# Performance work log

Measured on AMD Instinct MI355X. Metric: run time of the kernel, lower is better.

## Reference

```python
import jax, jax.numpy as jnp
import numpy as np

CHUNK_SIZE = 1024  # module default chunk_size


def setup_inputs() -> dict:
    key = jax.random.key(0)
    kq, kk, kv = jax.random.split(key, 3)
    B, H, S, D = 2, 16, 2048, 64
    q = jax.random.normal(kq, (B, H, S, D), dtype=jnp.float32)
    k = jax.random.normal(kk, (B, H, S, D), dtype=jnp.float32)
    v = jax.random.normal(kv, (B, H, S, D), dtype=jnp.float32)
    return {"q": q, "k": k, "v": v}


def reference(q, k, v):
    # Chunked causal attention: q split into chunks of CHUNK_SIZE along seq,
    # each chunk attends to the full K/V with causal mask (tril, diagonal=start).
    B, H, S, D = q.shape
    scale = D ** (-0.5)
    cs = CHUNK_SIZE
    nc = S // cs  # S is a multiple of chunk_size here
    qc = q.reshape(B, H, nc, cs, D)
    # scores: [B, H, nc, cs, S]
    scores = jnp.einsum('bhncd,bhsd->bhncs', qc, k) * scale
    # causal mask per chunk: key position j visible iff j <= chunk_start + i
    row = (jnp.arange(nc) * cs)[:, None, None] + jnp.arange(cs)[None, :, None]  # [nc, cs, 1]
    col = jnp.arange(S)[None, None, :]  # [1, 1, S]
    causal = col <= row  # [nc, cs, S]
    scores = jnp.where(causal[None, None], scores, -jnp.inf)
    attn = jax.nn.softmax(scores, axis=-1)
    out = jnp.einsum('bhncs,bhsd->bhncd', attn, v)
    return out.reshape(B, H, S, D)
```

## Files before the change

kernel.cpp:

```cpp
#include <hip/hip_runtime.h>

typedef __bf16 bf16x8 __attribute__((ext_vector_type(8)));
typedef float f32x4 __attribute__((ext_vector_type(4)));
typedef float f32x16 __attribute__((ext_vector_type(16)));

#define S_LEN 2048
#define D_DIM 64
#define NHEAD 32
#define PART_FLOATS 8448

typedef __attribute__((address_space(1))) const void gas;
typedef __attribute__((address_space(3))) void las;

#define J(c, t0, nt) ((unsigned short)((c) | ((t0) << 4) | ((nt) << 9)))
__device__ const unsigned short TRIP[24] = {
    J(15,0,16), J(15,16,16), J(0,0,2),
    J(7,0,16),  J(13,0,14),  J(1,0,4),
    J(14,0,15), J(12,0,13),  J(2,0,6),
    J(14,15,15),J(10,0,11),  J(3,0,8),
    J(13,14,14),J(10,11,11), J(8,0,9),
    J(6,0,14),  J(9,0,10),   J(9,10,10),
    J(12,13,13),J(11,0,12),  J(8,9,9),
    J(11,12,12),J(5,0,12),   J(4,0,10),
};

__global__ __launch_bounds__(256) void convert_kv(const float* __restrict__ K,
                                                  const float* __restrict__ V,
                                                  __bf16* __restrict__ Kb,
                                                  __bf16* __restrict__ Vtg) {
    const int head = blockIdx.y;
    const int s0   = blockIdx.x * 64;
    const int tr   = threadIdx.x >> 2;
    const int tc   = (threadIdx.x & 3) << 4;
    const size_t ib = (size_t)head * (S_LEN * D_DIM) + (size_t)(s0 + tr) * D_DIM + tc;

    __shared__ __bf16 tb[64][72];

    {
        const float* kr = K + ib;
        f32x4 a = *(const f32x4*)kr, b = *(const f32x4*)(kr + 4),
              c = *(const f32x4*)(kr + 8), d = *(const f32x4*)(kr + 12);
        bf16x8 o0, o1;
        #pragma unroll
        for (int e = 0; e < 4; ++e) {
            o0[e] = (__bf16)a[e]; o0[e + 4] = (__bf16)b[e];
            o1[e] = (__bf16)c[e]; o1[e + 4] = (__bf16)d[e];
        }
        __bf16* ko = Kb + ib;
        *(bf16x8*)ko = o0; *(bf16x8*)(ko + 8) = o1;
    }
    {
        const float* vr = V + ib;
        f32x4 a = *(const f32x4*)vr, b = *(const f32x4*)(vr + 4),
              c = *(const f32x4*)(vr + 8), d = *(const f32x4*)(vr + 12);
        #pragma unroll
        for (int e = 0; e < 4; ++e) {
            tb[tc +  e][tr] = (__bf16)a[e];
            tb[tc + 4 + e][tr] = (__bf16)b[e];
            tb[tc + 8 + e][tr] = (__bf16)c[e];
            tb[tc + 12 + e][tr] = (__bf16)d[e];
        }
    }
    __syncthreads();
    {
        bf16x8 o0, o1;
        #pragma unroll
        for (int e = 0; e < 8; ++e) { o0[e] = tb[tr][tc + e]; o1[e] = tb[tr][tc + 8 + e]; }
        __bf16* vo = Vtg + (size_t)head * (D_DIM * S_LEN) + (size_t)tr * S_LEN + s0 + tc;
        *(bf16x8*)vo = o0; *(bf16x8*)(vo + 8) = o1;
    }
}

__global__ __launch_bounds__(256, 3) void attn32(const float* __restrict__ Q,
                                                 const __bf16* __restrict__ Kb,
                                                 const __bf16* __restrict__ Vg,
                                                 float* __restrict__ O,
                                                 float* __restrict__ Pp) {
    const int b    = blockIdx.x;
    const int xcd  = b & 7;
    const int cu   = (b >> 3) & 31;
    const int pass = b >> 8;
    const int head = xcd * 4 + (cu >> 3);
    const unsigned short jw = TRIP[(cu & 7) * 3 + pass];
    const int chunk = jw & 15;
    const int t0    = (jw >> 4) & 31;
    const int nt    = jw >> 9;

    const int tid  = threadIdx.x;
    const int wave = tid >> 6;
    const int lane = tid & 63;
    const int l31  = lane & 31;
    const int hi   = lane >> 5;
    const int sw31 = (l31 & 7) << 3;

    const int q0w = chunk * 128 + wave * 32;
    const size_t qbase = (size_t)head * (S_LEN * D_DIM);
    const size_t vbase = (size_t)head * (D_DIM * S_LEN);
    const float qscale = 0.125f * 1.44269504088896340736f;

    __shared__ __align__(16) __bf16 Klds[2][64][64];
    __shared__ __align__(16) __bf16 Vt[2][64][64];

    const int xsw = (lane & 7) ^ ((lane >> 3) & 7);
    const size_t kOff = (size_t)(lane >> 3) * D_DIM + (size_t)xsw * 8;
    const size_t vOff = (size_t)(lane >> 3) * S_LEN + (size_t)xsw * 8;
    const __bf16* kgw = Kb + qbase + (size_t)(wave * 16) * D_DIM + kOff;
    const __bf16* vgw = Vg + vbase + (size_t)(wave * 16) * S_LEN + vOff;

    bf16x8 qf[4];
    {
        const float* qrow = Q + qbase + (size_t)(q0w + l31) * D_DIM + hi * 8;
        #pragma unroll
        for (int kd = 0; kd < 4; ++kd) {
            f32x4 a = *(const f32x4*)(qrow + kd * 16);
            f32x4 c = *(const f32x4*)(qrow + kd * 16 + 4);
            bf16x8 t;
            #pragma unroll
            for (int e = 0; e < 4; ++e) { t[e] = (__bf16)(a[e] * qscale); t[e + 4] = (__bf16)(c[e] * qscale); }
            qf[kd] = t;
        }
    }

    f32x16 acc0 = {0.f}, acc1 = {0.f};
    #pragma unroll
    for (int r = 0; r < 16; ++r) { acc0[r] = 0.f; acc1[r] = 0.f; }
    float m_r = -1e30f, l_r = 0.f;

    auto stage = [&](int kv0, int bufi) {
        const __bf16* kg = kgw + (size_t)kv0 * D_DIM;
        const __bf16* vg = vgw + kv0;
        __builtin_amdgcn_global_load_lds((gas*)kg,               (las*)&Klds[bufi][wave * 16][0],     16, 0, 0);
        __builtin_amdgcn_global_load_lds((gas*)(kg + 8 * D_DIM), (las*)&Klds[bufi][wave * 16 + 8][0], 16, 0, 0);
        __builtin_amdgcn_global_load_lds((gas*)vg,               (las*)&Vt[bufi][wave * 16][0],       16, 0, 0);
        __builtin_amdgcn_global_load_lds((gas*)(vg + 8 * S_LEN), (las*)&Vt[bufi][wave * 16 + 8][0],   16, 0, 0);
    };
    auto cvtpk = [](float lo, float hh) {
        unsigned int r;
        asm("v_cvt_pk_bf16_f32 %0, %1, %2" : "=v"(r) : "v"(lo), "v"(hh));
        return r;
    };

    stage(t0 << 6, 0);

    for (int it = 0; it < nt; ++it) {
        const int cur = it & 1;
        asm volatile("s_waitcnt vmcnt(0)" ::: "memory");
        __syncthreads();

        if (it + 1 < nt) stage((t0 + it + 1) << 6, cur ^ 1);
        const int kv0 = (t0 + it) << 6;

        if (kv0 <= q0w + 31) {
            f32x16 s0, s1;
            #pragma unroll
            for (int r = 0; r < 16; ++r) { s0[r] = 0.f; s1[r] = 0.f; }
            __builtin_amdgcn_s_setprio(1);
            #pragma unroll
            for (int kd = 0; kd < 4; ++kd) {
                bf16x8 kf0 = *(const bf16x8*)&Klds[cur][l31][(kd * 16 + hi * 8) ^ sw31];
                bf16x8 kf1 = *(const bf16x8*)&Klds[cur][32 + l31][(kd * 16 + hi * 8) ^ sw31];
                s0 = __builtin_amdgcn_mfma_f32_32x32x16_bf16(kf0, qf[kd], s0, 0, 0, 0);
                s1 = __builtin_amdgcn_mfma_f32_32x32x16_bf16(kf1, qf[kd], s1, 0, 0, 0);
            }
            __builtin_amdgcn_s_setprio(0);

            if (kv0 + 63 > q0w) {
                const int qg = q0w + l31;
                #pragma unroll
                for (int r = 0; r < 16; ++r) {
                    const int cr = (r & 3) + 8 * (r >> 2) + 4 * hi;
                    if (kv0 + cr > qg)      s0[r] = -1e30f;
                    if (kv0 + 32 + cr > qg) s1[r] = -1e30f;
                }
            }

            float mm = -1e30f;
            #pragma unroll
            for (int r = 0; r < 16; ++r) mm = fmaxf(mm, fmaxf(s0[r], s1[r]));
            mm = fmaxf(mm, __shfl_xor(mm, 32));
            if (!__all(mm - m_r <= 8.0f)) {
                const float mn = fmaxf(m_r, mm);
                const float f = exp2f(m_r - mn);
                m_r = mn;
                l_r *= f;
                #pragma unroll
                for (int r = 0; r < 16; ++r) {
                    const float fr = __shfl(f, (r & 3) + 8 * (r >> 2) + 4 * hi);
                    acc0[r] *= fr; acc1[r] *= fr;
                }
            }
            float ps = 0.f, ps2 = 0.f;
            #pragma unroll
            for (int r = 0; r < 16; ++r) {
                s0[r] = exp2f(s0[r] - m_r); ps  += s0[r];
                s1[r] = exp2f(s1[r] - m_r); ps2 += s1[r];
            }
            ps += ps2;
            ps += __shfl_xor(ps, 32);
            l_r += ps;

            __builtin_amdgcn_s_setprio(1);
            {
                unsigned int w01 = cvtpk(s0[0],  s0[1]),  w23 = cvtpk(s0[2],  s0[3]);
                unsigned int w45 = cvtpk(s0[4],  s0[5]),  w67 = cvtpk(s0[6],  s0[7]);
                unsigned int w89 = cvtpk(s0[8],  s0[9]),  wab = cvtpk(s0[10], s0[11]);
                unsigned int wcd = cvtpk(s0[12], s0[13]), wef = cvtpk(s0[14], s0[15]);
                asm("v_permlane32_swap_b32 %0, %1" : "+v"(w01), "+v"(w45));
                asm("v_permlane32_swap_b32 %0, %1" : "+v"(w23), "+v"(w67));
                asm("v_permlane32_swap_b32 %0, %1" : "+v"(w89), "+v"(wcd));
                asm("v_permlane32_swap_b32 %0, %1" : "+v"(wab), "+v"(wef));
                union { unsigned int u[4]; bf16x8 v; } f0 = {{w01, w23, w45, w67}};
                union { unsigned int u[4]; bf16x8 v; } f1 = {{w89, wab, wcd, wef}};
                bf16x8 v00 = *(const bf16x8*)&Vt[cur][l31][(hi * 8) ^ sw31];
                bf16x8 v01 = *(const bf16x8*)&Vt[cur][32 + l31][(hi * 8) ^ sw31];
                acc0 = __builtin_amdgcn_mfma_f32_32x32x16_bf16(f0.v, v00, acc0, 0, 0, 0);
                acc1 = __builtin_amdgcn_mfma_f32_32x32x16_bf16(f0.v, v01, acc1, 0, 0, 0);
                bf16x8 v10 = *(const bf16x8*)&Vt[cur][l31][(16 + hi * 8) ^ sw31];
                bf16x8 v11 = *(const bf16x8*)&Vt[cur][32 + l31][(16 + hi * 8) ^ sw31];
                acc0 = __builtin_amdgcn_mfma_f32_32x32x16_bf16(f1.v, v10, acc0, 0, 0, 0);
                acc1 = __builtin_amdgcn_mfma_f32_32x32x16_bf16(f1.v, v11, acc1, 0, 0, 0);
            }
            {
                unsigned int w01 = cvtpk(s1[0],  s1[1]),  w23 = cvtpk(s1[2],  s1[3]);
                unsigned int w45 = cvtpk(s1[4],  s1[5]),  w67 = cvtpk(s1[6],  s1[7]);
                unsigned int w89 = cvtpk(s1[8],  s1[9]),  wab = cvtpk(s1[10], s1[11]);
                unsigned int wcd = cvtpk(s1[12], s1[13]), wef = cvtpk(s1[14], s1[15]);
                asm("v_permlane32_swap_b32 %0, %1" : "+v"(w01), "+v"(w45));
                asm("v_permlane32_swap_b32 %0, %1" : "+v"(w23), "+v"(w67));
                asm("v_permlane32_swap_b32 %0, %1" : "+v"(w89), "+v"(wcd));
                asm("v_permlane32_swap_b32 %0, %1" : "+v"(wab), "+v"(wef));
                union { unsigned int u[4]; bf16x8 v; } f2 = {{w01, w23, w45, w67}};
                union { unsigned int u[4]; bf16x8 v; } f3 = {{w89, wab, wcd, wef}};
                bf16x8 v20 = *(const bf16x8*)&Vt[cur][l31][(32 + hi * 8) ^ sw31];
                bf16x8 v21 = *(const bf16x8*)&Vt[cur][32 + l31][(32 + hi * 8) ^ sw31];
                acc0 = __builtin_amdgcn_mfma_f32_32x32x16_bf16(f2.v, v20, acc0, 0, 0, 0);
                acc1 = __builtin_amdgcn_mfma_f32_32x32x16_bf16(f2.v, v21, acc1, 0, 0, 0);
                bf16x8 v30 = *(const bf16x8*)&Vt[cur][l31][(48 + hi * 8) ^ sw31];
                bf16x8 v31 = *(const bf16x8*)&Vt[cur][32 + l31][(48 + hi * 8) ^ sw31];
                acc0 = __builtin_amdgcn_mfma_f32_32x32x16_bf16(f3.v, v30, acc0, 0, 0, 0);
                acc1 = __builtin_amdgcn_mfma_f32_32x32x16_bf16(f3.v, v31, acc1, 0, 0, 0);
            }
            __builtin_amdgcn_s_setprio(0);
        }
    }

    if (chunk < 8) {
        const float inv_own = 1.0f / l_r;
        float* ob = O + qbase + (size_t)(chunk * 128 + wave * 32) * D_DIM + l31;
        #pragma unroll
        for (int r = 0; r < 16; ++r) {
            const int cr = (r & 3) + 8 * (r >> 2) + 4 * hi;
            const float inv = __shfl(inv_own, cr);
            ob[(size_t)cr * D_DIM]      = acc0[r] * inv;
            ob[(size_t)cr * D_DIM + 32] = acc1[r] * inv;
        }
    } else {
        const int seg = (t0 != 0) ? 1 : 0;
        float* pp = Pp + (size_t)((head * 8 + (chunk - 8)) * 2 + seg) * PART_FLOATS;
        if (hi == 0) {
            pp[wave * 32 + l31] = m_r;
            pp[128 + wave * 32 + l31] = l_r;
        }
        float* pb = pp + 256 + (size_t)(wave * 32) * 64 + l31;
        #pragma unroll
        for (int r = 0; r < 16; ++r) {
            const int cr = (r & 3) + 8 * (r >> 2) + 4 * hi;
            pb[(size_t)cr * 64]      = acc0[r];
            pb[(size_t)cr * 64 + 32] = acc1[r];
        }
    }
}

__global__ __launch_bounds__(256) void combine(const float* __restrict__ Pp,
                                               float* __restrict__ O) {
    const int head = blockIdx.y;
    const int ch   = blockIdx.x;
    const float* PA = Pp + (size_t)((head * 8 + ch) * 2) * PART_FLOATS;
    const float* PB = PA + PART_FLOATS;
    const int row = threadIdx.x >> 1;
    const int c0  = (threadIdx.x & 1) << 5;

    const float mA = PA[row], lA = PA[128 + row];
    const float mB = PB[row], lB = PB[128 + row];
    const float M  = fmaxf(mA, mB);
    const float wA = exp2f(mA - M), wB = exp2f(mB - M);
    const float inv = 1.0f / (lA * wA + lB * wB);

    const float* a = PA + 256 + (size_t)row * 64 + c0;
    const float* b = PB + 256 + (size_t)row * 64 + c0;
    float* o = O + (size_t)head * (S_LEN * D_DIM) + (size_t)((8 + ch) * 128 + row) * D_DIM + c0;
    #pragma unroll
    for (int i = 0; i < 8; ++i) {
        f32x4 va = *(const f32x4*)(a + 4 * i);
        f32x4 vb = *(const f32x4*)(b + 4 * i);
        f32x4 vo;
        #pragma unroll
        for (int e = 0; e < 4; ++e) vo[e] = (va[e] * wA + vb[e] * wB) * inv;
        *(f32x4*)(o + 4 * i) = vo;
    }
}

__global__ __launch_bounds__(256, 4) void attn_fwd_fb(const float* __restrict__ Q,
                                                      const float* __restrict__ K,
                                                      const float* __restrict__ V,
                                                      float* __restrict__ O) {
    const int b    = blockIdx.x;
    const int xcd  = b & 7;
    const int cs   = (b >> 3) & 31;
    const int j    = b >> 8;
    const int head = xcd * 4 + (cs >> 3);
    const int slot = cs & 7;
    const int chunk = (j == 0) ? slot : (j == 1) ? (31 - slot)
                    : (j == 2) ? (slot + 8) : (23 - slot);

    const int tid  = threadIdx.x;
    const int wave = tid >> 6;
    const int lane = tid & 63;
    const int l15  = lane & 15;
    const int lhi  = lane >> 4;

    const int q0 = chunk * 64 + wave * 16;
    const size_t base = (size_t)head * (S_LEN * D_DIM);
    const float qscale = 0.125f * 1.44269504088896340736f;

    __shared__ __align__(16) __bf16 Klds[2][64][64];
    __shared__ __align__(16) __bf16 Vt[2][64][64];
    __shared__ __align__(16) __bf16 Plds[4][16][64];

    const int rk = tid >> 2;
    const int ck = (tid & 3) << 4;
    const int kp = tid & 31;
    const int dc = tid >> 5;
    const int swk = (rk & 7) << 3;

    bf16x8 qf[2];
    {
        const float* qrow = Q + base + (size_t)(q0 + l15) * D_DIM + lhi * 8;
        #pragma unroll
        for (int h = 0; h < 2; ++h) {
            f32x4 a = *(const f32x4*)(qrow + h * 32);
            f32x4 bq = *(const f32x4*)(qrow + h * 32 + 4);
            bf16x8 t;
            #pragma unroll
            for (int e = 0; e < 4; ++e) { t[e] = (__bf16)(a[e] * qscale); t[e + 4] = (__bf16)(bq[e] * qscale); }
            qf[h] = t;
        }
    }

    f32x4 acc[4];
    #pragma unroll
    for (int td = 0; td < 4; ++td) acc[td] = (f32x4){0.f, 0.f, 0.f, 0.f};
    float m_r = -1e30f, l_r = 0.f;

    f32x4 pk[4], pva[2], pvb[2];
    {
        const float* ks = K + base + (size_t)rk * D_DIM + ck;
        #pragma unroll
        for (int i = 0; i < 4; ++i) pk[i] = *(const f32x4*)(ks + 4 * i);
        const float* v0 = V + base + (size_t)(2 * kp) * D_DIM + dc * 8;
        pva[0] = *(const f32x4*)v0;           pva[1] = *(const f32x4*)(v0 + 4);
        pvb[0] = *(const f32x4*)(v0 + D_DIM); pvb[1] = *(const f32x4*)(v0 + D_DIM + 4);
        bf16x8 k0, k1;
        #pragma unroll
        for (int e = 0; e < 4; ++e) {
            k0[e] = (__bf16)pk[0][e]; k0[e + 4] = (__bf16)pk[1][e];
            k1[e] = (__bf16)pk[2][e]; k1[e + 4] = (__bf16)pk[3][e];
        }
        *(bf16x8*)&Klds[0][rk][ck ^ swk] = k0;
        *(bf16x8*)&Klds[0][rk][(ck + 8) ^ swk] = k1;
        #pragma unroll
        for (int jj = 0; jj < 8; ++jj) {
            const int d = dc * 8 + jj;
            const float av = (jj < 4) ? pva[0][jj & 3] : pva[1][jj & 3];
            const float bv = (jj < 4) ? pvb[0][jj & 3] : pvb[1][jj & 3];
            union { __bf16 h[2]; unsigned int u; } t;
            t.h[0] = (__bf16)av; t.h[1] = (__bf16)bv;
            *(unsigned int*)&Vt[0][d][(2 * kp) ^ ((d & 7) << 3)] = t.u;
        }
    }

    const int nt = chunk + 1;
    for (int kt = 0; kt < nt; ++kt) {
        const int cur = kt & 1;
        __syncthreads();
        const bool pre = (kt + 1 < nt);
        if (pre) {
            const int kv1 = (kt + 1) << 6;
            const float* ks = K + base + (size_t)(kv1 + rk) * D_DIM + ck;
            #pragma unroll
            for (int i = 0; i < 4; ++i) pk[i] = *(const f32x4*)(ks + 4 * i);
            const float* v0 = V + base + (size_t)(kv1 + 2 * kp) * D_DIM + dc * 8;
            pva[0] = *(const f32x4*)v0;           pva[1] = *(const f32x4*)(v0 + 4);
            pvb[0] = *(const f32x4*)(v0 + D_DIM); pvb[1] = *(const f32x4*)(v0 + D_DIM + 4);
        }

        f32x4 s[4];
        #pragma unroll
        for (int ct = 0; ct < 4; ++ct) s[ct] = (f32x4){0.f, 0.f, 0.f, 0.f};
        #pragma unroll
        for (int h = 0; h < 2; ++h) {
            #pragma unroll
            for (int ct = 0; ct < 4; ++ct) {
                const int krow = ct * 16 + l15;
                bf16x8 kf = *(const bf16x8*)&Klds[cur][krow][(h * 32 + lhi * 8) ^ ((l15 & 7) << 3)];
                s[ct] = __builtin_amdgcn_mfma_f32_16x16x32_bf16(kf, qf[h], s[ct], 0, 0, 0);
            }
        }

        if (kt == nt - 1) {
            const int kv0 = kt << 6;
            const int qg = q0 + l15;
            #pragma unroll
            for (int ct = 0; ct < 4; ++ct)
                #pragma unroll
                for (int r = 0; r < 4; ++r) {
                    const int kg = kv0 + ct * 16 + lhi * 4 + r;
                    if (kg > qg) s[ct][r] = -1e30f;
                }
        }

        float mm = fmaxf(fmaxf(fmaxf(s[0][0], s[0][1]), fmaxf(s[0][2], s[0][3])),
                         fmaxf(fmaxf(s[1][0], s[1][1]), fmaxf(s[1][2], s[1][3])));
        mm = fmaxf(mm, fmaxf(fmaxf(fmaxf(s[2][0], s[2][1]), fmaxf(s[2][2], s[2][3])),
                             fmaxf(fmaxf(s[3][0], s[3][1]), fmaxf(s[3][2], s[3][3]))));
        mm = fmaxf(mm, __shfl_xor(mm, 16));
        mm = fmaxf(mm, __shfl_xor(mm, 32));
        if (!__all(mm - m_r <= 8.0f)) {
            const float mn = fmaxf(m_r, mm);
            const float f = exp2f(m_r - mn);
            m_r = mn;
            l_r *= f;
            #pragma unroll
            for (int r = 0; r < 4; ++r) {
                const float fr = __shfl(f, lhi * 4 + r);
                #pragma unroll
                for (int td = 0; td < 4; ++td) acc[td][r] *= fr;
            }
        }
        float ps = 0.f;
        #pragma unroll
        for (int ct = 0; ct < 4; ++ct)
            #pragma unroll
            for (int r = 0; r < 4; ++r) {
                const float p = exp2f(s[ct][r] - m_r);
                s[ct][r] = p;
                ps += p;
            }
        ps += __shfl_xor(ps, 16);
        ps += __shfl_xor(ps, 32);
        l_r += ps;

        #pragma unroll
        for (int ct = 0; ct < 4; ++ct) {
            union { __bf16 h[4]; unsigned long long u; } pw;
            #pragma unroll
            for (int r = 0; r < 4; ++r) pw.h[r] = (__bf16)s[ct][r];
            *(unsigned long long*)&Plds[wave][l15][(ct * 16 + lhi * 4) ^ ((l15 & 7) << 3)] = pw.u;
        }
        asm volatile("s_waitcnt lgkmcnt(0)" ::: "memory");
        bf16x8 pf[2];
        #pragma unroll
        for (int kh = 0; kh < 2; ++kh)
            pf[kh] = *(const bf16x8*)&Plds[wave][l15][(kh * 32 + lhi * 8) ^ ((l15 & 7) << 3)];
        asm volatile("" ::: "memory");

        #pragma unroll
        for (int kh = 0; kh < 2; ++kh) {
            #pragma unroll
            for (int td = 0; td < 4; ++td) {
                const int vrow = td * 16 + l15;
                bf16x8 vf = *(const bf16x8*)&Vt[cur][vrow][(kh * 32 + lhi * 8) ^ ((vrow & 7) << 3)];
                acc[td] = __builtin_amdgcn_mfma_f32_16x16x32_bf16(pf[kh], vf, acc[td], 0, 0, 0);
            }
        }

        if (pre) {
            const int nxt = cur ^ 1;
            bf16x8 k0, k1;
            #pragma unroll
            for (int e = 0; e < 4; ++e) {
                k0[e] = (__bf16)pk[0][e]; k0[e + 4] = (__bf16)pk[1][e];
                k1[e] = (__bf16)pk[2][e]; k1[e + 4] = (__bf16)pk[3][e];
            }
            *(bf16x8*)&Klds[nxt][rk][ck ^ swk] = k0;
            *(bf16x8*)&Klds[nxt][rk][(ck + 8) ^ swk] = k1;
            #pragma unroll
            for (int jj = 0; jj < 8; ++jj) {
                const int d = dc * 8 + jj;
                const float av = (jj < 4) ? pva[0][jj & 3] : pva[1][jj & 3];
                const float bv = (jj < 4) ? pvb[0][jj & 3] : pvb[1][jj & 3];
                union { __bf16 h[2]; unsigned int u; } t;
                t.h[0] = (__bf16)av; t.h[1] = (__bf16)bv;
                *(unsigned int*)&Vt[nxt][d][(2 * kp) ^ ((d & 7) << 3)] = t.u;
            }
        }
    }

    float* orow = O + base + (size_t)q0 * D_DIM;
    #pragma unroll
    for (int r = 0; r < 4; ++r) {
        const float inv = 1.0f / __shfl(l_r, lhi * 4 + r);
        #pragma unroll
        for (int td = 0; td < 4; ++td)
            orow[(size_t)(lhi * 4 + r) * D_DIM + td * 16 + l15] = acc[td][r] * inv;
    }
}

extern "C" void kernel_launch(void* const* d_in, const int* in_sizes, int n_in,
                              void* d_out, int out_size, void* d_ws, size_t ws_size,
                              hipStream_t stream) {
    const float* q = (const float*)d_in[0];
    const float* k = (const float*)d_in[1];
    const float* v = (const float*)d_in[2];
    float* o = (float*)d_out;
    const size_t elems = (size_t)NHEAD * S_LEN * D_DIM;
    const size_t kvBytes = 2 * elems * sizeof(__bf16);
    const size_t partBytes = (size_t)512 * PART_FLOATS * sizeof(float);
    if (ws_size >= kvBytes + partBytes) {
        __bf16* Kb  = (__bf16*)d_ws;
        __bf16* Vtg = Kb + elems;
        float* Pp   = (float*)((char*)d_ws + kvBytes);
        convert_kv<<<dim3(32, 32), dim3(256), 0, stream>>>(k, v, Kb, Vtg);
        attn32<<<dim3(768), dim3(256), 0, stream>>>(q, Kb, Vtg, o, Pp);
        combine<<<dim3(8, 32), dim3(256), 0, stream>>>(Pp, o);
    } else {
        attn_fwd_fb<<<dim3(1024), dim3(256), 0, stream>>>(q, k, v, o);
    }
}
```

Before: 62.68 us.

## Split causal KV work into five balanced jobs per CU with multi-segment combine

Replaces the three-job-per-CU schedule with a five-job table where long query chunks are split into KV segments of at most eight tiles, launching 1280 blocks at higher occupancy (launch bound 5). The combine kernel is generalised to merge 2–4 partial segments per chunk using log-sum-exp weights. It also rewrites the row max and sum reductions as tree reductions to shorten dependency chains. The aim is better load balance and latency hiding across CUs, at the cost of more partial writes and a heavier combine step.

```diff
diff --git a/kernel.cpp b/kernel.cpp
--- a/kernel.cpp
+++ b/kernel.cpp
@@ -13,6 +13,20 @@
 typedef __attribute__((address_space(3))) void las;
 
 #define J(c, t0, nt) ((unsigned short)((c) | ((t0) << 4) | ((nt) << 9)))
+
+__device__ const unsigned short JOBS5[40] = {
+    J(15,0,8), J(15,8,8), J(15,16,8), J(15,24,8), J(0,0,2),
+    J(14,0,8), J(14,8,8), J(14,16,8), J(13,16,8), J(4,8,2),
+    J(13,0,8), J(13,8,8), J(12,16,8), J(12,8,8),  J(8,16,2),
+    J(12,0,8), J(11,16,8),J(11,8,8),  J(11,0,8),  J(12,24,2),
+    J(10,0,8), J(10,8,8), J(9,8,8),   J(1,0,4),   J(10,16,6),
+    J(9,0,8),  J(8,8,8),  J(8,0,8),   J(5,8,4),   J(14,24,6),
+    J(7,8,8),  J(7,0,8),  J(6,0,8),   J(9,16,4),  J(6,8,6),
+    J(5,0,8),  J(4,0,8),  J(3,0,8),   J(13,24,4), J(2,0,6),
+};
+__device__ const int PRE[12]  = {0,2,4,6,8,11,14,17,20,24,28,32};
+__device__ const int NSEG[12] = {2,2,2,2,3,3,3,3,4,4,4,4};
+
 __device__ const unsigned short TRIP[24] = {
     J(15,0,16), J(15,16,16), J(0,0,2),
     J(7,0,16),  J(13,0,14),  J(1,0,4),
@@ -71,17 +85,20 @@
     }
 }
 
-__global__ __launch_bounds__(256, 3) void attn32(const float* __restrict__ Q,
-                                                 const __bf16* __restrict__ Kb,
-                                                 const __bf16* __restrict__ Vg,
-                                                 float* __restrict__ O,
-                                                 float* __restrict__ Pp) {
+template <int MODE>
+__global__ __launch_bounds__(256, MODE == 0 ? 5 : 3)
+void attn32(const float* __restrict__ Q,
+            const __bf16* __restrict__ Kb,
+            const __bf16* __restrict__ Vg,
+            float* __restrict__ O,
+            float* __restrict__ Pp) {
     const int b    = blockIdx.x;
     const int xcd  = b & 7;
     const int cu   = (b >> 3) & 31;
     const int pass = b >> 8;
     const int head = xcd * 4 + (cu >> 3);
-    const unsigned short jw = TRIP[(cu & 7) * 3 + pass];
+    const unsigned short jw = (MODE == 0) ? JOBS5[(cu & 7) * 5 + pass]
+                                          : TRIP[(cu & 7) * 3 + pass];
     const int chunk = jw & 15;
     const int t0    = (jw >> 4) & 31;
     const int nt    = jw >> 9;
@@ -121,7 +138,7 @@
         }
     }
 
-    f32x16 acc0 = {0.f}, acc1 = {0.f};
+    f32x16 acc0, acc1;
     #pragma unroll
     for (int r = 0; r < 16; ++r) { acc0[r] = 0.f; acc1[r] = 0.f; }
     float m_r = -1e30f, l_r = 0.f;
@@ -174,10 +191,14 @@
                 }
             }
 
-            float mm = -1e30f;
-            #pragma unroll
-            for (int r = 0; r < 16; ++r) mm = fmaxf(mm, fmaxf(s0[r], s1[r]));
-            mm = fmaxf(mm, __shfl_xor(mm, 32));
+            float t[16];
+            #pragma unroll
+            for (int r = 0; r < 16; ++r) t[r] = fmaxf(s0[r], s1[r]);
+            #pragma unroll
+            for (int off = 8; off >= 1; off >>= 1)
+                #pragma unroll
+                for (int r = 0; r < 16; ++r) if (r < off) t[r] = fmaxf(t[r], t[r + off]);
+            float mm = fmaxf(t[0], __shfl_xor(t[0], 32));
             if (!__all(mm - m_r <= 8.0f)) {
                 const float mn = fmaxf(m_r, mm);
                 const float f = exp2f(m_r - mn);
@@ -189,15 +210,18 @@
                     acc0[r] *= fr; acc1[r] *= fr;
                 }
             }
-            float ps = 0.f, ps2 = 0.f;
+            float u[16];
             #pragma unroll
             for (int r = 0; r < 16; ++r) {
-                s0[r] = exp2f(s0[r] - m_r); ps  += s0[r];
-                s1[r] = exp2f(s1[r] - m_r); ps2 += s1[r];
-            }
-            ps += ps2;
-            ps += __shfl_xor(ps, 32);
-            l_r += ps;
+                s0[r] = exp2f(s0[r] - m_r);
+                s1[r] = exp2f(s1[r] - m_r);
+                u[r] = s0[r] + s1[r];
+            }
+            #pragma unroll
+            for (int off = 8; off >= 1; off >>= 1)
+                #pragma unroll
+                for (int r = 0; r < 16; ++r) if (r < off) u[r] += u[r + off];
+            l_r += u[0] + __shfl_xor(u[0], 32);
 
             __builtin_amdgcn_s_setprio(1);
             {
@@ -244,7 +268,8 @@
         }
     }
 
-    if (chunk < 8) {
+    const bool direct = (MODE == 0) ? (chunk < 4) : (chunk < 8);
+    if (direct) {
         const float inv_own = 1.0f / l_r;
         float* ob = O + qbase + (size_t)(chunk * 128 + wave * 32) * D_DIM + l31;
         #pragma unroll
@@ -255,8 +280,10 @@
             ob[(size_t)cr * D_DIM + 32] = acc1[r] * inv;
         }
     } else {
-        const int seg = (t0 != 0) ? 1 : 0;
-        float* pp = Pp + (size_t)((head * 8 + (chunk - 8)) * 2 + seg) * PART_FLOATS;
+        size_t slot;
+        if (MODE == 0) slot = (size_t)head * 36 + PRE[chunk - 4] + (t0 >> 3);
+        else           slot = (size_t)((head * 8 + (chunk - 8)) * 2 + (t0 != 0 ? 1 : 0));
+        float* pp = Pp + slot * PART_FLOATS;
         if (hi == 0) {
             pp[wave * 32 + l31] = m_r;
             pp[128 + wave * 32 + l31] = l_r;
@@ -271,31 +298,47 @@
     }
 }
 
+template <int MODE>
 __global__ __launch_bounds__(256) void combine(const float* __restrict__ Pp,
                                                float* __restrict__ O) {
     const int head = blockIdx.y;
-    const int ch   = blockIdx.x;
-    const float* PA = Pp + (size_t)((head * 8 + ch) * 2) * PART_FLOATS;
-    const float* PB = PA + PART_FLOATS;
+    const int bx   = blockIdx.x;
+    const int ch   = (MODE == 0) ? (4 + bx) : (8 + bx);
+    const int ns   = (MODE == 0) ? NSEG[bx] : 2;
+    const size_t base = (MODE == 0) ? ((size_t)head * 36 + PRE[bx])
+                                    : (size_t)((head * 8 + bx) * 2);
     const int row = threadIdx.x >> 1;
     const int c0  = (threadIdx.x & 1) << 5;
 
-    const float mA = PA[row], lA = PA[128 + row];
-    const float mB = PB[row], lB = PB[128 + row];
-    const float M  = fmaxf(mA, mB);
-    const float wA = exp2f(mA - M), wB = exp2f(mB - M);
-    const float inv = 1.0f / (lA * wA + lB * wB);
-
-    const float* a = PA + 256 + (size_t)row * 64 + c0;
-    const float* b = PB + 256 + (size_t)row * 64 + c0;
-    float* o = O + (size_t)head * (S_LEN * D_DIM) + (size_t)((8 + ch) * 128 + row) * D_DIM + c0;
+    float m[4], l[4], w[4];
+    float M = -1e30f;
+    #pragma unroll
+    for (int s = 0; s < 4; ++s)
+        if (s < ns) {
+            const float* P = Pp + (base + s) * PART_FLOATS;
+            m[s] = P[row]; l[s] = P[128 + row];
+            M = fmaxf(M, m[s]);
+        }
+    float L = 0.f;
+    #pragma unroll
+    for (int s = 0; s < 4; ++s)
+        if (s < ns) { w[s] = exp2f(m[s] - M); L += l[s] * w[s]; }
+    const float inv = 1.0f / L;
+
+    float* o = O + (size_t)head * (S_LEN * D_DIM) + (size_t)(ch * 128 + row) * D_DIM + c0;
     #pragma unroll
     for (int i = 0; i < 8; ++i) {
-        f32x4 va = *(const f32x4*)(a + 4 * i);
-        f32x4 vb = *(const f32x4*)(b + 4 * i);
-        f32x4 vo;
-        #pragma unroll
-        for (int e = 0; e < 4; ++e) vo[e] = (va[e] * wA + vb[e] * wB) * inv;
+        f32x4 vo = (f32x4){0.f, 0.f, 0.f, 0.f};
+        #pragma unroll
+        for (int s = 0; s < 4; ++s)
+            if (s < ns) {
+                const float* a = Pp + (base + s) * PART_FLOATS + 256 + (size_t)row * 64 + c0;
+                f32x4 va = *(const f32x4*)(a + 4 * i);
+                #pragma unroll
+                for (int e = 0; e < 4; ++e) vo[e] += va[e] * w[s];
+            }
+        #pragma unroll
+        for (int e = 0; e < 4; ++e) vo[e] *= inv;
         *(f32x4*)(o + 4 * i) = vo;
     }
 }
@@ -515,14 +558,22 @@
     float* o = (float*)d_out;
     const size_t elems = (size_t)NHEAD * S_LEN * D_DIM;
     const size_t kvBytes = 2 * elems * sizeof(__bf16);
-    const size_t partBytes = (size_t)512 * PART_FLOATS * sizeof(float);
-    if (ws_size >= kvBytes + partBytes) {
+    const size_t partA = (size_t)NHEAD * 36 * PART_FLOATS * sizeof(float);
+    const size_t partB = (size_t)512 * PART_FLOATS * sizeof(float);
+    if (ws_size >= kvBytes + partA) {
         __bf16* Kb  = (__bf16*)d_ws;
         __bf16* Vtg = Kb + elems;
         float* Pp   = (float*)((char*)d_ws + kvBytes);
         convert_kv<<<dim3(32, 32), dim3(256), 0, stream>>>(k, v, Kb, Vtg);
-        attn32<<<dim3(768), dim3(256), 0, stream>>>(q, Kb, Vtg, o, Pp);
-        combine<<<dim3(8, 32), dim3(256), 0, stream>>>(Pp, o);
+        attn32<0><<<dim3(1280), dim3(256), 0, stream>>>(q, Kb, Vtg, o, Pp);
+        combine<0><<<dim3(12, 32), dim3(256), 0, stream>>>(Pp, o);
+    } else if (ws_size >= kvBytes + partB) {
+        __bf16* Kb  = (__bf16*)d_ws;
+        __bf16* Vtg = Kb + elems;
+        float* Pp   = (float*)((char*)d_ws + kvBytes);
+        convert_kv<<<dim3(32, 32), dim3(256), 0, stream>>>(k, v, Kb, Vtg);
+        attn32<1><<<dim3(768), dim3(256), 0, stream>>>(q, Kb, Vtg, o, Pp);
+        combine<1><<<dim3(8, 32), dim3(256), 0, stream>>>(Pp, o);
     } else {
         attn_fwd_fb<<<dim3(1024), dim3(256), 0, stream>>>(q, k, v, o);
     }
```

Result: slower. 113.7 us (+81.4%).
